# Optimization experiments

Measured on AMD Instinct MI355X. Metric: run time of the kernel, lower is better.

The kernel has to match this reference:

```python
import jax, jax.numpy as jnp
import numpy as np

B, D, H, W, C = 1, 6, 128, 128, 180
NH = 6
HD = C // NH
SCALE = HD ** -0.5
WS = (2, 8, 8)
SS = (1, 4, 4)
N = WS[0] * WS[1] * WS[2]  # 128 tokens per 3D window
HID = int(C * 2.0)  # GEGLU hidden = 360


def _rel_pos_index(ws):
    d, h, w = np.meshgrid(np.arange(ws[0]), np.arange(ws[1]), np.arange(ws[2]), indexing='ij')
    coords = np.stack([d, h, w]).reshape(3, -1)  # (3, N)
    rel = (coords[:, :, None] - coords[:, None, :]).transpose(1, 2, 0).astype(np.int64)
    rel[:, :, 0] += ws[0] - 1
    rel[:, :, 1] += ws[1] - 1
    rel[:, :, 2] += ws[2] - 1
    rel[:, :, 0] *= (2 * ws[1] - 1) * (2 * ws[2] - 1)
    rel[:, :, 1] *= (2 * ws[2] - 1)
    return rel.sum(-1).astype(np.int32)  # (N, N)


def _sine_pos(hw, nf, temperature=10000.0):
    scale = 2.0 * np.pi
    ones = np.ones((1, hw[0], hw[1]), np.float64)
    y = np.cumsum(ones, 1)
    x = np.cumsum(ones, 2)
    eps = 1e-6
    y = y / (y[:, -1:, :] + eps) * scale
    x = x / (x[:, :, -1:] + eps) * scale
    dim_t = temperature ** (2 * (np.arange(nf) // 2) / nf)
    px = x[..., None] / dim_t
    py = y[..., None] / dim_t
    px = np.stack([np.sin(px[..., 0::2]), np.cos(px[..., 1::2])], -1).reshape(1, hw[0], hw[1], -1)
    py = np.stack([np.sin(py[..., 0::2]), np.cos(py[..., 1::2])], -1).reshape(1, hw[0], hw[1], -1)
    pos = np.concatenate([py, px], -1)  # (1, H, W, 2*nf)
    return pos.reshape(1, hw[0] * hw[1], -1).astype(np.float32)


def _compute_mask():
    img = np.zeros((1, D, H, W, 1), np.float32)
    cnt = 0
    sl = lambda w, s: (slice(0, -w), slice(-w, -s), slice(-s, None))
    for ds in sl(WS[0], SS[0]):
        for hs in sl(WS[1], SS[1]):
            for ws_ in sl(WS[2], SS[2]):
                img[:, ds, hs, ws_, :] = cnt
                cnt += 1
    mw = img.reshape(1, D // WS[0], WS[0], H // WS[1], WS[1], W // WS[2], WS[2], 1)
    mw = mw.transpose(0, 1, 3, 5, 2, 4, 6, 7).reshape(-1, N)
    am = mw[:, None, :] - mw[:, :, None]
    return np.where(am != 0, -100.0, 0.0).astype(np.float32)  # (nW, N, N)


def win_part(x):
    b = x.shape[0]
    x = x.reshape(b, D // WS[0], WS[0], H // WS[1], WS[1], W // WS[2], WS[2], C)
    return x.transpose(0, 1, 3, 5, 2, 4, 6, 7).reshape(-1, N, C)


def win_rev(w, b):
    x = w.reshape(b, D // WS[0], H // WS[1], W // WS[2], WS[0], WS[1], WS[2], C)
    return x.transpose(0, 1, 4, 2, 5, 3, 6, 7).reshape(b, D, H, W, C)


def ln(x, g, b):
    m = x.mean(-1, keepdims=True)
    v = ((x - m) ** 2).mean(-1, keepdims=True)
    return (x - m) / jnp.sqrt(v + 1e-5) * g + b


def attn_fn(q, k, v, bias, mask):
    # q,k,v: (B_, NH, n, HD); bias: (NH, n, n) or None; mask: (nW, n, n) or None
    a = jnp.einsum('bhnd,bhmd->bhnm', q * SCALE, k)
    if bias is not None:
        a = a + bias[None]
    if mask is not None:
        nW = mask.shape[0]
        a = a.reshape(-1, nW, NH, a.shape[-2], a.shape[-1]) + mask[None, :, None]
        a = a.reshape(-1, NH, a.shape[-2], a.shape[-1])
    a = jax.nn.softmax(a, axis=-1)
    o = jnp.einsum('bhnm,bhmd->bhnd', a, v)
    return o.transpose(0, 2, 1, 3).reshape(o.shape[0], o.shape[2], -1)


def setup_inputs() -> dict:
    key = jax.random.key(0)
    ks = jax.random.split(key, 9)
    p = lambda k, shape: jax.random.normal(k, shape, jnp.float32) * 0.02
    return {
        'x': jax.random.normal(ks[0], (B, D, H, W, C), jnp.float32),
        'mask': jnp.asarray(_compute_mask()),
        'g1': jnp.ones((C,), jnp.float32), 'b1': jnp.zeros((C,), jnp.float32),
        'g2': jnp.ones((C,), jnp.float32), 'b2': jnp.zeros((C,), jnp.float32),
        'w_qkv_self': p(ks[1], (C, 3 * C)), 'b_qkv_self': jnp.zeros((3 * C,), jnp.float32),
        'w_qkv_mut': p(ks[2], (C, 3 * C)), 'b_qkv_mut': jnp.zeros((3 * C,), jnp.float32),
        'rpb_table': p(ks[3], ((2 * WS[0] - 1) * (2 * WS[1] - 1) * (2 * WS[2] - 1), NH)),
        'pos_bias': jnp.asarray(_sine_pos((WS[1], WS[2]), C // 2)),
        'w_proj': p(ks[4], (2 * C, C)), 'b_proj': jnp.zeros((C,), jnp.float32),
        'w_fc11': p(ks[5], (C, HID)), 'b_fc11': jnp.zeros((HID,), jnp.float32),
        'w_fc12': p(ks[6], (C, HID)), 'b_fc12': jnp.zeros((HID,), jnp.float32),
        'w_fc2': p(ks[7], (HID, C)), 'b_fc2': jnp.zeros((C,), jnp.float32),
        'rpi': jnp.asarray(_rel_pos_index(WS)),
    }


def reference(x, mask, g1, b1, g2, b2, w_qkv_self, b_qkv_self, w_qkv_mut, b_qkv_mut,
              rpb_table, pos_bias, w_proj, b_proj, w_fc11, b_fc11, w_fc12, b_fc12,
              w_fc2, b_fc2, rpi):
    # --- attention branch ---
    h = ln(x, g1, b1)
    h = jnp.roll(h, (-SS[0], -SS[1], -SS[2]), axis=(1, 2, 3))  # cyclic shift
    xw = win_part(h)  # (B*nW, N, C)
    B_ = xw.shape[0]

    def qkv(xin, wq, bq):
        t = (xin @ wq + bq).reshape(B_, -1, 3, NH, HD).transpose(2, 0, 3, 1, 4)
        return t[0], t[1], t[2]

    q, k, v = qkv(xw, w_qkv_self, b_qkv_self)
    bias = rpb_table[rpi.reshape(-1)].reshape(N, N, NH).transpose(2, 0, 1)
    x_self = attn_fn(q, k, v, bias, mask)

    # mutual attention between the two frames of each window
    pb = jnp.concatenate([pos_bias, pos_bias], axis=1)  # (1, N, C)
    qm, km, vm = qkv(xw + pb, w_qkv_mut, b_qkv_mut)
    half = N // 2
    q1, q2 = qm[:, :, :half], qm[:, :, half:]
    k1, k2 = km[:, :, :half], km[:, :, half:]
    v1, v2 = vm[:, :, :half], vm[:, :, half:]
    m2 = mask[:, :half, :half]
    x1 = attn_fn(q2, k1, v1, None, m2)
    x2 = attn_fn(q1, k2, v2, None, m2)
    xo = jnp.concatenate([jnp.concatenate([x1, x2], axis=1), x_self], axis=2)  # (B_, N, 2C)
    xo = xo @ w_proj + b_proj
    out = win_rev(xo, x.shape[0])
    out = jnp.roll(out, (SS[0], SS[1], SS[2]), axis=(1, 2, 3))
    x = x + out

    # --- GEGLU MLP branch ---
    h = ln(x, g2, b2)
    h = jax.nn.gelu(h @ w_fc11 + b_fc11, approximate=False) * (h @ w_fc12 + b_fc12)
    x = x + (h @ w_fc2 + b_fc2)
    return x
```

## Files before the change

### kernel.cpp

```cpp
#include <hip/hip_runtime.h>
#include <hip/hip_bf16.h>
#include <math.h>
#include <cstdio>


typedef __hip_bfloat16 bf16;
typedef __attribute__((ext_vector_type(8))) short short8;
typedef __attribute__((ext_vector_type(4))) unsigned short us4;
typedef __attribute__((ext_vector_type(4))) float f32x4;

#define SCALE_F 0.18257418583505536f
#define SZPE 18874368u

__device__ __forceinline__ bf16  f2b(float v){ return __float2bfloat16(v); }
__device__ __forceinline__ float bu2f(unsigned short u){
    union { unsigned int i; float f; } x; x.i = ((unsigned int)u) << 16; return x.f;
}
__device__ __forceinline__ f32x4 mfma16(short8 a, short8 b, f32x4 c){
    return __builtin_amdgcn_mfma_f32_16x16x32_bf16(a, b, c, 0, 0, 0);
}

__device__ __forceinline__ void gld16(const bf16* g, bf16* s){
    __builtin_amdgcn_global_load_lds(
        (const __attribute__((address_space(1))) unsigned int*)g,
        (__attribute__((address_space(3))) unsigned int*)s, 16, 0, 0);
}

__device__ __forceinline__ float gelu_erf(float x){
    float z  = fabsf(x) * 0.70710678118654752f;
    float t  = __builtin_amdgcn_rcpf(fmaf(0.3275911f, z, 1.f));
    float p  = fmaf(fmaf(fmaf(fmaf(1.061405429f, t, -1.453152027f),
                              t, 1.421413741f), t, -0.284496736f), t, 0.254829592f) * t;
    float e  = __expf(-z * z);
    float er = fmaf(-p, e, 1.f);
    er = (x >= 0.f) ? er : -er;
    return 0.5f * x * (1.f + er);
}

__device__ __forceinline__ int xswz(){
    return (blockIdx.x & 7) * ((int)gridDim.x >> 3) + ((int)blockIdx.x >> 3);
}

__device__ __forceinline__ int wincnt(int win, int tok){
    int d = (win >> 8) * 2 + (tok >> 6);
    int h = ((win >> 4) & 15) * 8 + ((tok >> 3) & 7);
    int w = (win & 15) * 8 + (tok & 7);
    int rd = (d >= 4) + (d >= 5);
    int rh = (h >= 120) + (h >= 124);
    int rw = (w >= 120) + (w >= 124);
    return (rd * 3 + rh) * 3 + rw;
}

__device__ __forceinline__ size_t wrev_base(int row){
    int win = row >> 7, tok = row & 127;
    int wd = win >> 8, wh = (win >> 4) & 15, ww = win & 15;
    int td = tok >> 6, th = (tok >> 3) & 7, tw = tok & 7;
    int d = wd * 2 + td + 1; if (d >= 6) d -= 6;
    int h = (wh * 8 + th + 4) & 127;
    int wcol = (ww * 8 + tw + 4) & 127;
    return ((size_t)((d * 128 + h) * 128 + wcol)) * 180;
}

__global__ __launch_bounds__(256) void k_pack_qkv(const float* __restrict__ w,
                                                  const float* __restrict__ bias,
                                                  bf16* __restrict__ Bt,
                                                  float* __restrict__ bb)
{
    int idx = blockIdx.x * 256 + threadIdx.x;
    int n = idx / 192, k = idx - n * 192;
    int three = n / 192;
    int rem = n - three * 192, nh = rem >> 5, hdp = rem & 31;
    int srcc = three * 180 + nh * 30 + hdp;
    float v = 0.f;
    if (hdp < 30 && k < 180) v = w[(size_t)k * 540 + srcc];
    if (three == 0) v *= SCALE_F;
    Bt[(size_t)n * 192 + k] = f2b(v);
    if (k == 0) bb[n] = (hdp < 30) ? ((three == 0 ? SCALE_F : 1.f) * bias[srcc]) : 0.f;
}

__global__ __launch_bounds__(256) void k_pack(const float* __restrict__ w,
                                              int NW, int K, int KP,
                                              bf16* __restrict__ Bt)
{
    int idx = blockIdx.x * 256 + threadIdx.x;
    int n = idx / KP, k = idx - n * KP;
    float v = (n < NW && k < K) ? w[(size_t)k * NW + n] : 0.f;
    Bt[idx] = f2b(v);
}

__global__ __launch_bounds__(256) void k_rpbg(const float* __restrict__ rpb,
                                              const int* __restrict__ rpi,
                                              bf16* __restrict__ biasrT)
{
    int n = blockIdx.x * 256 + threadIdx.x;
    int nh = n >> 14, rc = n & 16383;
    int row = rc >> 7, col = rc & 127;
    biasrT[((size_t)nh * 128 + col) * 128 + row] = f2b(rpb[rpi[rc] * 6 + nh]);
}

__global__ __launch_bounds__(256) void k_zpad(bf16* __restrict__ attn)
{
    int gi = blockIdx.x * 256 + threadIdx.x;
    int row = gi / 3, part = gi - row * 3;
    *(uint4*)&attn[(size_t)row * 384 + 360 + part * 8] = make_uint4(0u,0u,0u,0u);
}

template<bool ROLL_PB>
__global__ __launch_bounds__(256) void k_ln(const float* __restrict__ x,
                                            const float* __restrict__ g,
                                            const float* __restrict__ b,
                                            const float* __restrict__ pb,
                                            bf16* __restrict__ xw,
                                            bf16* __restrict__ xwm)
{
    int row  = blockIdx.x * 4 + (threadIdx.x >> 6);
    int lane = threadIdx.x & 63;
    const float* src;
    if (ROLL_PB) {
        src = x + wrev_base(row) - 0;
    } else {
        src = x + (size_t)row * 180;
    }
    float v0 = src[lane];
    float v1 = src[lane + 64];
    float v2 = (lane < 52) ? src[lane + 128] : 0.f;
    float s  = v0 + v1 + v2;
    float ss = v0*v0 + v1*v1 + v2*v2;
    #pragma unroll
    for (int o = 32; o > 0; o >>= 1) { s += __shfl_xor(s, o, 64); ss += __shfl_xor(ss, o, 64); }
    float mean = s * (1.f/180.f);
    float var  = ss * (1.f/180.f) - mean*mean;
    float rstd = rsqrtf(var + 1e-5f);

    bf16* dst = xw + (size_t)row * 192;
    float y0 = (v0-mean)*rstd*g[lane]     + b[lane];
    float y1 = (v1-mean)*rstd*g[lane+64]  + b[lane+64];
    float y2 = (lane < 52) ? ((v2-mean)*rstd*g[lane+128] + b[lane+128]) : 0.f;
    dst[lane]      = f2b(y0);
    dst[lane+64]   = f2b(y1);
    if (lane < 52) dst[lane+128] = f2b(y2);
    if (lane < 12) dst[180+lane] = f2b(0.f);
    if (ROLL_PB) {
        const float* pbr = pb + (size_t)(row & 63) * 180;
        bf16* dm = xwm + (size_t)row * 192;
        dm[lane]      = f2b(y0 + pbr[lane]);
        dm[lane+64]   = f2b(y1 + pbr[lane+64]);
        if (lane < 52) dm[lane+128] = f2b(y2 + pbr[lane+128]);
        if (lane < 12) dm[180+lane] = f2b(0.f);
    }
}

template<int KP, bool DUAL>
__device__ __forceinline__ void mm2(const bf16* __restrict__ A,
                                    const bf16* __restrict__ Bt1,
                                    const bf16* __restrict__ Bt2,
                                    bf16* As, bf16* Bs1, bf16* Bs2,
                                    int m0, int n0,
                                    f32x4 (&acc1)[2][4], f32x4 (&acc2)[2][4])
{
    const int tid = threadIdx.x;
    const int w = tid >> 6, l = tid & 63, q = l >> 4, c = l & 15;
    const int lr = l >> 3, lj = l & 7;
    const int swz = ((lj ^ lr) << 3);
    #pragma unroll
    for (int ks = 0; ks < KP / 64; ks++) {
        #pragma unroll
        for (int e = 0; e < 4; e++) {
            int m = (e * 4 + w) * 8 + lr;
            gld16(&A[(size_t)(m0 + m) * KP + ks * 64 + swz], &As[((e * 4 + w) * 8) * 64]);
        }
        #pragma unroll
        for (int e = 0; e < 2; e++) {
            int n = (e * 4 + w) * 8 + lr;
            gld16(&Bt1[(size_t)(n0 + n) * KP + ks * 64 + swz], &Bs1[((e * 4 + w) * 8) * 64]);
            if (DUAL)
                gld16(&Bt2[(size_t)(n0 + n) * KP + ks * 64 + swz], &Bs2[((e * 4 + w) * 8) * 64]);
        }
        __syncthreads();
        #pragma unroll
        for (int k32 = 0; k32 < 2; k32++) {
            int koff = (((k32 * 4 + q) ^ (c & 7)) << 3);
            short8 a[2];
            #pragma unroll
            for (int mt = 0; mt < 2; mt++)
                a[mt] = *(const short8*)&As[(w * 32 + mt * 16 + c) * 64 + koff];
            #pragma unroll
            for (int nt = 0; nt < 4; nt++) {
                short8 b1 = *(const short8*)&Bs1[(nt * 16 + c) * 64 + koff];
                #pragma unroll
                for (int mt = 0; mt < 2; mt++) acc1[mt][nt] = mfma16(a[mt], b1, acc1[mt][nt]);
                if (DUAL) {
                    short8 b2 = *(const short8*)&Bs2[(nt * 16 + c) * 64 + koff];
                    #pragma unroll
                    for (int mt = 0; mt < 2; mt++) acc2[mt][nt] = mfma16(a[mt], b2, acc2[mt][nt]);
                }
            }
        }
        __syncthreads();
    }
}

__device__ __forceinline__ int cs_idx(int row, int colt){
    return row * 64 + ((((colt >> 3) ^ ((row >> 2) & 7)) << 3) | (colt & 7));
}

__global__ __launch_bounds__(256) void k_qkv(const bf16* __restrict__ A,
                                             const bf16* __restrict__ Bt,
                                             const float* __restrict__ bb,
                                             bf16* __restrict__ outq)
{
    __shared__ __align__(16) bf16 As[128 * 64];
    __shared__ __align__(16) bf16 Bs[64 * 64];
    int bid = xswz();
    int n0 = (bid % 9) * 64, m0 = (bid / 9) * 128;
    f32x4 a1[2][4] = {}, a2[2][4];
    mm2<192, false>(A, Bt, nullptr, As, Bs, nullptr, m0, n0, a1, a2);

    int tid = threadIdx.x, w = tid >> 6, l = tid & 63, q = l >> 4, c = l & 15;
    bf16* Cs = As;
    #pragma unroll
    for (int mt = 0; mt < 2; mt++)
      #pragma unroll
      for (int nt = 0; nt < 4; nt++)
        #pragma unroll
        for (int r = 0; r < 4; r++) {
            int row = w * 32 + mt * 16 + q * 4 + r;
            int colt = nt * 16 + c;
            Cs[cs_idx(row, colt)] = f2b(a1[mt][nt][r] + bb[n0 + colt]);
        }
    __syncthreads();
    int win = m0 >> 7;
    #pragma unroll
    for (int e = 0; e < 4; e++) {
        int gi = e * 256 + tid;
        int row = gi >> 3, j = gi & 7, c8 = j * 8;
        int col = n0 + c8;
        int three = col / 192, rem = col - three * 192;
        int nh = rem >> 5, hdp = rem & 31;
        bf16* dst = outq + (size_t)three * SZPE + ((size_t)(win * 6 + nh) * 128 + row) * 32 + hdp;
        *(uint4*)dst = *(const uint4*)&Cs[row * 64 + ((j ^ ((row >> 2) & 7)) << 3)];
    }
}

__global__ __launch_bounds__(256) void k_proj(const bf16* __restrict__ A,
                                              const bf16* __restrict__ Bt,
                                              const float* __restrict__ bias,
                                              const float* __restrict__ xin,
                                              float* __restrict__ res)
{
    __shared__ __align__(16) char smem[24576];
    bf16*  As = (bf16*)smem;
    bf16*  Bs = (bf16*)(smem + 16384);
    float* Cs = (float*)smem;
    int bid = xswz();
    int n0 = (bid % 3) * 64, m0 = (bid / 3) * 128;
    f32x4 a1[2][4] = {}, a2[2][4];
    mm2<384, false>(A, Bt, nullptr, As, Bs, nullptr, m0, n0, a1, a2);

    int tid = threadIdx.x, w = tid >> 6, l = tid & 63, q = l >> 4, c = l & 15;
    #pragma unroll
    for (int h = 0; h < 2; h++) {
        __syncthreads();
        if ((w >> 1) == h) {
            #pragma unroll
            for (int mt = 0; mt < 2; mt++)
              #pragma unroll
              for (int nt = 0; nt < 4; nt++)
                #pragma unroll
                for (int r = 0; r < 4; r++) {
                    int rl = (w & 1) * 32 + mt * 16 + q * 4 + r;
                    Cs[rl * 76 + nt * 16 + c] = a1[mt][nt][r];
                }
        }
        __syncthreads();
        #pragma unroll
        for (int e = 0; e < 4; e++) {
            int slot = e * 256 + tid;
            int rl = slot >> 4, cq = slot & 15;
            int col = n0 + cq * 4;
            if (col < 180) {
                size_t base = wrev_base(m0 + h * 64 + rl) + col;
                float4 xi = *(const float4*)&xin[base];
                float4 bi = *(const float4*)&bias[col];
                const float* cp = &Cs[rl * 76 + cq * 4];
                float4 o;
                o.x = xi.x + cp[0] + bi.x;
                o.y = xi.y + cp[1] + bi.y;
                o.z = xi.z + cp[2] + bi.z;
                o.w = xi.w + cp[3] + bi.w;
                *(float4*)&res[base] = o;
            }
        }
    }
}

__global__ __launch_bounds__(256) void k_fc1(const bf16* __restrict__ A,
                                             const bf16* __restrict__ Bt1,
                                             const float* __restrict__ bb1,
                                             const bf16* __restrict__ Bt2,
                                             const float* __restrict__ bb2,
                                             bf16* __restrict__ hid)
{
    __shared__ __align__(16) bf16 As[128 * 64];
    __shared__ __align__(16) bf16 Bs1[64 * 64];
    __shared__ __align__(16) bf16 Bs2[64 * 64];
    int bid = xswz();
    int n0 = (bid % 6) * 64, m0 = (bid / 6) * 128;
    f32x4 a1[2][4] = {}, a2[2][4] = {};
    mm2<192, true>(A, Bt1, Bt2, As, Bs1, Bs2, m0, n0, a1, a2);

    int tid = threadIdx.x, w = tid >> 6, l = tid & 63, q = l >> 4, c = l & 15;
    bf16* Cs = As;
    #pragma unroll
    for (int mt = 0; mt < 2; mt++)
      #pragma unroll
      for (int nt = 0; nt < 4; nt++)
        #pragma unroll
        for (int r = 0; r < 4; r++) {
            int row = w * 32 + mt * 16 + q * 4 + r;
            int colt = nt * 16 + c;
            int col = n0 + colt;
            float hv = 0.f;
            if (col < 360)
                hv = gelu_erf(a1[mt][nt][r] + bb1[col]) * (a2[mt][nt][r] + bb2[col]);
            Cs[cs_idx(row, colt)] = f2b(hv);
        }
    __syncthreads();
    #pragma unroll
    for (int e = 0; e < 4; e++) {
        int gi = e * 256 + tid;
        int row = gi >> 3, j = gi & 7, c8 = j * 8;
        *(uint4*)&hid[(size_t)(m0 + row) * 384 + n0 + c8] =
            *(const uint4*)&Cs[row * 64 + ((j ^ ((row >> 2) & 7)) << 3)];
    }
}

__global__ __launch_bounds__(256) void k_fc2(const bf16* __restrict__ A,
                                             const bf16* __restrict__ Bt,
                                             const float* __restrict__ bias,
                                             float* __restrict__ out)
{
    __shared__ __align__(16) char smem[24576];
    bf16*  As = (bf16*)smem;
    bf16*  Bs = (bf16*)(smem + 16384);
    float* Cs = (float*)smem;
    int bid = xswz();
    int n0 = (bid % 3) * 64, m0 = (bid / 3) * 128;
    f32x4 a1[2][4] = {}, a2[2][4];
    mm2<384, false>(A, Bt, nullptr, As, Bs, nullptr, m0, n0, a1, a2);

    int tid = threadIdx.x, w = tid >> 6, l = tid & 63, q = l >> 4, c = l & 15;
    #pragma unroll
    for (int h = 0; h < 2; h++) {
        __syncthreads();
        if ((w >> 1) == h) {
            #pragma unroll
            for (int mt = 0; mt < 2; mt++)
              #pragma unroll
              for (int nt = 0; nt < 4; nt++)
                #pragma unroll
                for (int r = 0; r < 4; r++) {
                    int rl = (w & 1) * 32 + mt * 16 + q * 4 + r;
                    Cs[rl * 76 + nt * 16 + c] = a1[mt][nt][r];
                }
        }
        __syncthreads();
        #pragma unroll
        for (int e = 0; e < 4; e++) {
            int slot = e * 256 + tid;
            int rl = slot >> 4, cq = slot & 15;
            int col = n0 + cq * 4;
            if (col < 180) {
                size_t idx = (size_t)(m0 + h * 64 + rl) * 180 + col;
                float4 ov = *(const float4*)&out[idx];
                float4 bi = *(const float4*)&bias[col];
                const float* cp = &Cs[rl * 76 + cq * 4];
                ov.x += cp[0] + bi.x;
                ov.y += cp[1] + bi.y;
                ov.z += cp[2] + bi.z;
                ov.w += cp[3] + bi.w;
                *(float4*)&out[idx] = ov;
            }
        }
    }
}

template<bool MUT>
__global__ __launch_bounds__(256) void k_attn(const bf16* __restrict__ qkv,
                                              const bf16* __restrict__ biasrT,
                                              bf16* __restrict__ aout)
{
    __shared__ __align__(16) bf16 Vts[32 * 136];
    __shared__ __align__(16) bf16 Ps[128 * 136];

    int wh = blockIdx.x, win = wh / 6, nh = wh - win * 6;
    const bf16* qg = qkv + (size_t)wh * 4096;
    const bf16* kg = qg + (size_t)SZPE;
    const bf16* vg = qg + 2 * (size_t)SZPE;
    int tid = threadIdx.x, w = tid >> 6, l = tid & 63, q = l >> 4, c = l & 15;

    #pragma unroll
    for (int e = 0; e < 2; e++) {
        int base = (e * 256 + tid) * 8;
        int tok = base >> 5, hd0 = base & 31;
        uint4 vv = *(const uint4*)&vg[base];
        const bf16* pv = (const bf16*)&vv;
        #pragma unroll
        for (int i = 0; i < 8; i++) {
            int hd = hd0 + i;
            Vts[hd * 136 + (tok ^ (((hd >> 3) & 3) << 3))] = pv[i];
        }
    }

    f32x4 S[2][8];
    #pragma unroll
    for (int mt = 0; mt < 2; mt++)
        #pragma unroll
        for (int nt = 0; nt < 8; nt++) S[mt][nt] = (f32x4){0.f, 0.f, 0.f, 0.f};
    {
        short8 a[2];
        #pragma unroll
        for (int mt = 0; mt < 2; mt++) {
            int rq = w * 32 + mt * 16 + c;
            if (MUT) rq ^= 64;
            a[mt] = *(const short8*)&qg[rq * 32 + q * 8];
        }
        #pragma unroll
        for (int nt = 0; nt < 8; nt++) {
            short8 b = *(const short8*)&kg[(nt * 16 + c) * 32 + q * 8];
            #pragma unroll
            for (int mt = 0; mt < 2; mt++) S[mt][nt] = mfma16(a[mt], b, S[mt][nt]);
        }
    }

    int rcnt[2][4], ccnt[8];
    #pragma unroll
    for (int mt = 0; mt < 2; mt++)
        #pragma unroll
        for (int r = 0; r < 4; r++) {
            int row = w * 32 + mt * 16 + q * 4 + r;
            rcnt[mt][r] = wincnt(win, MUT ? (row & 63) : row);
        }
    #pragma unroll
    for (int nt = 0; nt < 8; nt++) {
        int col = nt * 16 + c;
        ccnt[nt] = wincnt(win, MUT ? (col & 63) : col);
    }

    float mx[2][4];
    #pragma unroll
    for (int mt = 0; mt < 2; mt++)
      #pragma unroll
      for (int r = 0; r < 4; r++) mx[mt][r] = -3.0e38f;

    #pragma unroll
    for (int mt = 0; mt < 2; mt++)
      #pragma unroll
      for (int nt = 0; nt < 8; nt++) {
        float bv[4];
        if (!MUT) {
            int col = nt * 16 + c;
            us4 bb = *(const us4*)&biasrT[((size_t)(nh * 128 + col)) * 128
                                          + w * 32 + mt * 16 + q * 4];
            #pragma unroll
            for (int r = 0; r < 4; r++) bv[r] = bu2f(bb[r]);
        }
        bool valid = (w < 2) == (nt < 4);
        #pragma unroll
        for (int r = 0; r < 4; r++) {
            float s = S[mt][nt][r];
            if (MUT) {
                s = (rcnt[mt][r] == ccnt[nt]) ? s : s - 100.f;
                s = valid ? s : -30000.f;
            } else {
                s += bv[r];
                if (rcnt[mt][r] != ccnt[nt]) s -= 100.f;
            }
            S[mt][nt][r] = s;
            mx[mt][r] = fmaxf(mx[mt][r], s);
        }
      }
    #pragma unroll
    for (int mt = 0; mt < 2; mt++)
      #pragma unroll
      for (int r = 0; r < 4; r++) {
          float m = mx[mt][r];
          #pragma unroll
          for (int o = 1; o < 16; o <<= 1) m = fmaxf(m, __shfl_xor(m, o, 64));
          mx[mt][r] = m;
      }

    float sm[2][4] = {};
    #pragma unroll
    for (int mt = 0; mt < 2; mt++)
      #pragma unroll
      for (int nt = 0; nt < 8; nt++)
        #pragma unroll
        for (int r = 0; r < 4; r++) {
            float p = __expf(S[mt][nt][r] - mx[mt][r]);
            sm[mt][r] += p;
            Ps[(w * 32 + mt * 16 + q * 4 + r) * 136 + ((nt * 16 + c) ^ (q << 3))] = f2b(p);
        }
    #pragma unroll
    for (int mt = 0; mt < 2; mt++)
      #pragma unroll
      for (int r = 0; r < 4; r++) {
          float s = sm[mt][r];
          #pragma unroll
          for (int o = 1; o < 16; o <<= 1) s += __shfl_xor(s, o, 64);
          sm[mt][r] = s;
      }
    __syncthreads();

    f32x4 O[2][2];
    #pragma unroll
    for (int mt = 0; mt < 2; mt++)
        #pragma unroll
        for (int nt = 0; nt < 2; nt++) O[mt][nt] = (f32x4){0.f, 0.f, 0.f, 0.f};
    #pragma unroll
    for (int ks = 0; ks < 4; ks++) {
        short8 a[2];
        #pragma unroll
        for (int mt = 0; mt < 2; mt++) {
            int row = w * 32 + mt * 16 + c;
            int xr = ((c >> 2) & 3) << 3;
            a[mt] = *(const short8*)&Ps[row * 136 + (ks * 32 + ((q << 3) ^ xr))];
        }
        #pragma unroll
        for (int nt = 0; nt < 2; nt++) {
            int hd = nt * 16 + c;
            int xv = ((hd >> 3) & 3) << 3;
            short8 b = *(const short8*)&Vts[hd * 136 + (ks * 32 + ((q << 3) ^ xv))];
            #pragma unroll
            for (int mt = 0; mt < 2; mt++) O[mt][nt] = mfma16(a[mt], b, O[mt][nt]);
        }
    }

    #pragma unroll
    for (int mt = 0; mt < 2; mt++)
      #pragma unroll
      for (int r = 0; r < 4; r++) {
          int row = w * 32 + mt * 16 + q * 4 + r;
          float inv = 1.f / sm[mt][r];
          #pragma unroll
          for (int nt = 0; nt < 2; nt++) {
              int col = nt * 16 + c;
              if (col < 30)
                  aout[((size_t)win * 128 + row) * 384 + (MUT ? 0 : 180) + nh * 30 + col] =
                      f2b(O[mt][nt][r] * inv);
          }
      }
}

extern "C" void kernel_launch(void* const* d_in, const int* in_sizes, int n_in,
                              void* d_out, int out_size, void* d_ws, size_t ws_size,
                              hipStream_t stream)
{
    const float* x     = (const float*)d_in[0];
    const float* mask  = (const float*)d_in[1];
    const float* g1    = (const float*)d_in[2];
    const float* b1    = (const float*)d_in[3];
    const float* g2    = (const float*)d_in[4];
    const float* b2    = (const float*)d_in[5];
    const float* wqs   = (const float*)d_in[6];
    const float* bqs   = (const float*)d_in[7];
    const float* wqm   = (const float*)d_in[8];
    const float* bqm   = (const float*)d_in[9];
    const float* rpb   = (const float*)d_in[10];
    const float* posb  = (const float*)d_in[11];
    const float* wproj = (const float*)d_in[12];
    const float* bproj = (const float*)d_in[13];
    const float* w11   = (const float*)d_in[14];
    const float* bf11  = (const float*)d_in[15];
    const float* w12   = (const float*)d_in[16];
    const float* bf12  = (const float*)d_in[17];
    const float* w2    = (const float*)d_in[18];
    const float* bf2   = (const float*)d_in[19];
    const int*   rpi   = (const int*)d_in[20];
    float* out = (float*)d_out;
    (void)mask;

    const size_t need = 265671168;
    if (ws_size < need) { fprintf(stderr, "[tmsa] ws too small: %zu < %zu\n", ws_size, need); return; }

    char* W = (char*)d_ws;
    bf16*  xw     = (bf16*)W;
    bf16*  xwm    = (bf16*)(W + 37748736);
    bf16*  attn   = (bf16*)(W + 75497472);
    bf16*  qkv    = (bf16*)(W + 150994944);
    bf16*  biasrT = (bf16*)(W + 264241152);
    bf16*  Btqs   = (bf16*)(W + 264634368);
    bf16*  Btqm   = (bf16*)(W + 264855552);
    float* bbqs   = (float*)(W + 265076736);
    float* bbqm   = (float*)(W + 265079040);
    bf16*  Btproj = (bf16*)(W + 265081344);
    bf16*  Btf11  = (bf16*)(W + 265228800);
    bf16*  Btf12  = (bf16*)(W + 265376256);
    bf16*  Btf2   = (bf16*)(W + 265523712);

    k_rpbg<<<dim3(384), 256, 0, stream>>>(rpb, rpi, biasrT);
    k_pack_qkv<<<dim3(432), 256, 0, stream>>>(wqs, bqs, Btqs, bbqs);
    k_pack_qkv<<<dim3(432), 256, 0, stream>>>(wqm, bqm, Btqm, bbqm);
    k_pack<<<dim3(288), 256, 0, stream>>>(wproj, 180, 360, 384, Btproj);
    k_pack<<<dim3(288), 256, 0, stream>>>(w11,   360, 180, 192, Btf11);
    k_pack<<<dim3(288), 256, 0, stream>>>(w12,   360, 180, 192, Btf12);
    k_pack<<<dim3(288), 256, 0, stream>>>(w2,    180, 360, 384, Btf2);

    k_ln<true><<<dim3(24576), 256, 0, stream>>>(x, g1, b1, posb, xw, xwm);
    k_zpad<<<dim3(1152), 256, 0, stream>>>(attn);
    k_qkv<<<dim3(6912), 256, 0, stream>>>(xw, Btqs, bbqs, qkv);
    k_attn<false><<<dim3(4608), 256, 0, stream>>>(qkv, biasrT, attn);
    k_qkv<<<dim3(6912), 256, 0, stream>>>(xwm, Btqm, bbqm, qkv);
    k_attn<true><<<dim3(4608), 256, 0, stream>>>(qkv, biasrT, attn);
    k_proj<<<dim3(2304), 256, 0, stream>>>(attn, Btproj, bproj, x, out);
    k_ln<false><<<dim3(24576), 256, 0, stream>>>(out, g2, b2, nullptr, xw, nullptr);
    k_fc1<<<dim3(4608), 256, 0, stream>>>(xw, Btf11, bf11, Btf12, bf12, attn);
    k_fc2<<<dim3(2304), 256, 0, stream>>>(attn, Btf2, bf2, out);
}
```

Baseline: 590.9 us.

## Load GEMM operands directly from global memory into MFMA registers, dropping LDS staging

The shared GEMM helper used by the qkv, proj, fc1 and fc2 kernels no longer stages A and B tiles through LDS with async global-to-LDS loads and barriers. Each lane now reads its MFMA fragments straight from global memory. This removes the block-wide barriers and frees LDS, which may allow more blocks per CU. In exchange, B tiles are re-read by all four waves and each read is a strided 16-byte access, so the kernels lean on L1/L2 hit rates instead of explicit data reuse.

```diff
diff --git a/kernel.cpp b/kernel.cpp
--- a/kernel.cpp
+++ b/kernel.cpp
@@ -18,12 +18,6 @@
 }
 __device__ __forceinline__ f32x4 mfma16(short8 a, short8 b, f32x4 c){
     return __builtin_amdgcn_mfma_f32_16x16x32_bf16(a, b, c, 0, 0, 0);
-}
-
-__device__ __forceinline__ void gld16(const bf16* g, bf16* s){
-    __builtin_amdgcn_global_load_lds(
-        (const __attribute__((address_space(1))) unsigned int*)g,
-        (__attribute__((address_space(3))) unsigned int*)s, 16, 0, 0);
 }
 
 __device__ __forceinline__ float gelu_erf(float x){
@@ -117,7 +111,7 @@
     int lane = threadIdx.x & 63;
     const float* src;
     if (ROLL_PB) {
-        src = x + wrev_base(row) - 0;
+        src = x + wrev_base(row);
     } else {
         src = x + (size_t)row * 180;
     }
@@ -151,52 +145,33 @@
 }
 
 template<int KP, bool DUAL>
-__device__ __forceinline__ void mm2(const bf16* __restrict__ A,
+__device__ __forceinline__ void mm3(const bf16* __restrict__ A,
                                     const bf16* __restrict__ Bt1,
                                     const bf16* __restrict__ Bt2,
-                                    bf16* As, bf16* Bs1, bf16* Bs2,
                                     int m0, int n0,
                                     f32x4 (&acc1)[2][4], f32x4 (&acc2)[2][4])
 {
     const int tid = threadIdx.x;
     const int w = tid >> 6, l = tid & 63, q = l >> 4, c = l & 15;
-    const int lr = l >> 3, lj = l & 7;
-    const int swz = ((lj ^ lr) << 3);
-    #pragma unroll
-    for (int ks = 0; ks < KP / 64; ks++) {
-        #pragma unroll
-        for (int e = 0; e < 4; e++) {
-            int m = (e * 4 + w) * 8 + lr;
-            gld16(&A[(size_t)(m0 + m) * KP + ks * 64 + swz], &As[((e * 4 + w) * 8) * 64]);
-        }
-        #pragma unroll
-        for (int e = 0; e < 2; e++) {
-            int n = (e * 4 + w) * 8 + lr;
-            gld16(&Bt1[(size_t)(n0 + n) * KP + ks * 64 + swz], &Bs1[((e * 4 + w) * 8) * 64]);
-            if (DUAL)
-                gld16(&Bt2[(size_t)(n0 + n) * KP + ks * 64 + swz], &Bs2[((e * 4 + w) * 8) * 64]);
-        }
-        __syncthreads();
-        #pragma unroll
-        for (int k32 = 0; k32 < 2; k32++) {
-            int koff = (((k32 * 4 + q) ^ (c & 7)) << 3);
-            short8 a[2];
-            #pragma unroll
-            for (int mt = 0; mt < 2; mt++)
-                a[mt] = *(const short8*)&As[(w * 32 + mt * 16 + c) * 64 + koff];
-            #pragma unroll
-            for (int nt = 0; nt < 4; nt++) {
-                short8 b1 = *(const short8*)&Bs1[(nt * 16 + c) * 64 + koff];
-                #pragma unroll
-                for (int mt = 0; mt < 2; mt++) acc1[mt][nt] = mfma16(a[mt], b1, acc1[mt][nt]);
-                if (DUAL) {
-                    short8 b2 = *(const short8*)&Bs2[(nt * 16 + c) * 64 + koff];
-                    #pragma unroll
-                    for (int mt = 0; mt < 2; mt++) acc2[mt][nt] = mfma16(a[mt], b2, acc2[mt][nt]);
-                }
+    const bf16* a0p = A + (size_t)(m0 + w * 32 + c) * KP + q * 8;
+    const bf16* a1p = a0p + (size_t)16 * KP;
+    const bf16* bp  = Bt1 + (size_t)(n0 + c) * KP + q * 8;
+    const bf16* b2p = DUAL ? (Bt2 + (size_t)(n0 + c) * KP + q * 8) : nullptr;
+    #pragma unroll
+    for (int ks = 0; ks < KP / 32; ks++) {
+        short8 a0 = *(const short8*)(a0p + ks * 32);
+        short8 a1 = *(const short8*)(a1p + ks * 32);
+        #pragma unroll
+        for (int nt = 0; nt < 4; nt++) {
+            short8 b1 = *(const short8*)(bp + (size_t)(nt * 16) * KP + ks * 32);
+            acc1[0][nt] = mfma16(a0, b1, acc1[0][nt]);
+            acc1[1][nt] = mfma16(a1, b1, acc1[1][nt]);
+            if (DUAL) {
+                short8 b2 = *(const short8*)(b2p + (size_t)(nt * 16) * KP + ks * 32);
+                acc2[0][nt] = mfma16(a0, b2, acc2[0][nt]);
+                acc2[1][nt] = mfma16(a1, b2, acc2[1][nt]);
             }
         }
-        __syncthreads();
     }
 }
 
@@ -209,15 +184,13 @@
                                              const float* __restrict__ bb,
                                              bf16* __restrict__ outq)
 {
-    __shared__ __align__(16) bf16 As[128 * 64];
-    __shared__ __align__(16) bf16 Bs[64 * 64];
+    __shared__ __align__(16) bf16 Cs[128 * 64];
     int bid = xswz();
     int n0 = (bid % 9) * 64, m0 = (bid / 9) * 128;
     f32x4 a1[2][4] = {}, a2[2][4];
-    mm2<192, false>(A, Bt, nullptr, As, Bs, nullptr, m0, n0, a1, a2);
+    mm3<192, false>(A, Bt, nullptr, m0, n0, a1, a2);
 
     int tid = threadIdx.x, w = tid >> 6, l = tid & 63, q = l >> 4, c = l & 15;
-    bf16* Cs = As;
     #pragma unroll
     for (int mt = 0; mt < 2; mt++)
       #pragma unroll
@@ -248,14 +221,11 @@
                                               const float* __restrict__ xin,
                                               float* __restrict__ res)
 {
-    __shared__ __align__(16) char smem[24576];
-    bf16*  As = (bf16*)smem;
-    bf16*  Bs = (bf16*)(smem + 16384);
-    float* Cs = (float*)smem;
+    __shared__ __align__(16) float Cs[64 * 76];
     int bid = xswz();
     int n0 = (bid % 3) * 64, m0 = (bid / 3) * 128;
     f32x4 a1[2][4] = {}, a2[2][4];
-    mm2<384, false>(A, Bt, nullptr, As, Bs, nullptr, m0, n0, a1, a2);
+    mm3<384, false>(A, Bt, nullptr, m0, n0, a1, a2);
 
     int tid = threadIdx.x, w = tid >> 6, l = tid & 63, q = l >> 4, c = l & 15;
     #pragma unroll
@@ -301,16 +271,13 @@
                                              const float* __restrict__ bb2,
                                              bf16* __restrict__ hid)
 {
-    __shared__ __align__(16) bf16 As[128 * 64];
-    __shared__ __align__(16) bf16 Bs1[64 * 64];
-    __shared__ __align__(16) bf16 Bs2[64 * 64];
+    __shared__ __align__(16) bf16 Cs[128 * 64];
     int bid = xswz();
     int n0 = (bid % 6) * 64, m0 = (bid / 6) * 128;
     f32x4 a1[2][4] = {}, a2[2][4] = {};
-    mm2<192, true>(A, Bt1, Bt2, As, Bs1, Bs2, m0, n0, a1, a2);
+    mm3<192, true>(A, Bt1, Bt2, m0, n0, a1, a2);
 
     int tid = threadIdx.x, w = tid >> 6, l = tid & 63, q = l >> 4, c = l & 15;
-    bf16* Cs = As;
     #pragma unroll
     for (int mt = 0; mt < 2; mt++)
       #pragma unroll
@@ -340,14 +307,11 @@
                                              const float* __restrict__ bias,
                                              float* __restrict__ out)
 {
-    __shared__ __align__(16) char smem[24576];
-    bf16*  As = (bf16*)smem;
-    bf16*  Bs = (bf16*)(smem + 16384);
-    float* Cs = (float*)smem;
+    __shared__ __align__(16) float Cs[64 * 76];
     int bid = xswz();
     int n0 = (bid % 3) * 64, m0 = (bid / 3) * 128;
     f32x4 a1[2][4] = {}, a2[2][4];
-    mm2<384, false>(A, Bt, nullptr, As, Bs, nullptr, m0, n0, a1, a2);
+    mm3<384, false>(A, Bt, nullptr, m0, n0, a1, a2);
 
     int tid = threadIdx.x, w = tid >> 6, l = tid & 63, q = l >> 4, c = l & 15;
     #pragma unroll
```

After: 901.3 us. 1.53x slower.

## Double GEMM M-tile to 256 rows and vectorize layernorm loads/stores

Applied to the files above, without the earlier changes.

All four GEMM kernels (qkv, proj, fc1, fc2) now use 256-row tiles. Each wave computes 64 rows with a 4x4 MFMA accumulator grid, so each B tile loaded into LDS is reused across twice as many rows and the grid size is halved. The layernorm kernel switches to float4 loads and packed 4-wide bf16 stores instead of scalar per-lane accesses. The larger tiles raise register and LDS use (fc1 has dual 4x4 accumulators), which may reduce occupancy and latency hiding.

```diff
diff --git a/kernel.cpp b/kernel.cpp
--- a/kernel.cpp
+++ b/kernel.cpp
@@ -15,6 +15,13 @@
 __device__ __forceinline__ bf16  f2b(float v){ return __float2bfloat16(v); }
 __device__ __forceinline__ float bu2f(unsigned short u){
     union { unsigned int i; float f; } x; x.i = ((unsigned int)u) << 16; return x.f;
+}
+__device__ __forceinline__ us4 pack4(float a, float b, float c, float d){
+    us4 r;
+    bf16 t0 = f2b(a), t1 = f2b(b), t2 = f2b(c), t3 = f2b(d);
+    r[0] = *(unsigned short*)&t0; r[1] = *(unsigned short*)&t1;
+    r[2] = *(unsigned short*)&t2; r[3] = *(unsigned short*)&t3;
+    return r;
 }
 __device__ __forceinline__ f32x4 mfma16(short8 a, short8 b, f32x4 c){
     return __builtin_amdgcn_mfma_f32_16x16x32_bf16(a, b, c, 0, 0, 0);
@@ -115,17 +122,11 @@
 {
     int row  = blockIdx.x * 4 + (threadIdx.x >> 6);
     int lane = threadIdx.x & 63;
-    const float* src;
-    if (ROLL_PB) {
-        src = x + wrev_base(row) - 0;
-    } else {
-        src = x + (size_t)row * 180;
-    }
-    float v0 = src[lane];
-    float v1 = src[lane + 64];
-    float v2 = (lane < 52) ? src[lane + 128] : 0.f;
-    float s  = v0 + v1 + v2;
-    float ss = v0*v0 + v1*v1 + v2*v2;
+    const float* src = ROLL_PB ? (x + wrev_base(row)) : (x + (size_t)row * 180);
+    float4 v = make_float4(0.f, 0.f, 0.f, 0.f);
+    if (lane < 45) v = *(const float4*)&src[lane * 4];
+    float s  = v.x + v.y + v.z + v.w;
+    float ss = v.x*v.x + v.y*v.y + v.z*v.z + v.w*v.w;
     #pragma unroll
     for (int o = 32; o > 0; o >>= 1) { s += __shfl_xor(s, o, 64); ss += __shfl_xor(ss, o, 64); }
     float mean = s * (1.f/180.f);
@@ -133,30 +134,37 @@
     float rstd = rsqrtf(var + 1e-5f);
 
     bf16* dst = xw + (size_t)row * 192;
-    float y0 = (v0-mean)*rstd*g[lane]     + b[lane];
-    float y1 = (v1-mean)*rstd*g[lane+64]  + b[lane+64];
-    float y2 = (lane < 52) ? ((v2-mean)*rstd*g[lane+128] + b[lane+128]) : 0.f;
-    dst[lane]      = f2b(y0);
-    dst[lane+64]   = f2b(y1);
-    if (lane < 52) dst[lane+128] = f2b(y2);
-    if (lane < 12) dst[180+lane] = f2b(0.f);
+    float4 y = make_float4(0.f, 0.f, 0.f, 0.f);
+    if (lane < 45) {
+        float4 gv = *(const float4*)&g[lane * 4];
+        float4 bv = *(const float4*)&b[lane * 4];
+        y.x = (v.x - mean) * rstd * gv.x + bv.x;
+        y.y = (v.y - mean) * rstd * gv.y + bv.y;
+        y.z = (v.z - mean) * rstd * gv.z + bv.z;
+        y.w = (v.w - mean) * rstd * gv.w + bv.w;
+        *(us4*)&dst[lane * 4] = pack4(y.x, y.y, y.z, y.w);
+    } else if (lane < 48) {
+        *(us4*)&dst[lane * 4] = (us4){0, 0, 0, 0};
+    }
     if (ROLL_PB) {
-        const float* pbr = pb + (size_t)(row & 63) * 180;
         bf16* dm = xwm + (size_t)row * 192;
-        dm[lane]      = f2b(y0 + pbr[lane]);
-        dm[lane+64]   = f2b(y1 + pbr[lane+64]);
-        if (lane < 52) dm[lane+128] = f2b(y2 + pbr[lane+128]);
-        if (lane < 12) dm[180+lane] = f2b(0.f);
+        if (lane < 45) {
+            const float* pbr = pb + (size_t)(row & 63) * 180;
+            float4 pv = *(const float4*)&pbr[lane * 4];
+            *(us4*)&dm[lane * 4] = pack4(y.x + pv.x, y.y + pv.y, y.z + pv.z, y.w + pv.w);
+        } else if (lane < 48) {
+            *(us4*)&dm[lane * 4] = (us4){0, 0, 0, 0};
+        }
     }
 }
 
 template<int KP, bool DUAL>
-__device__ __forceinline__ void mm2(const bf16* __restrict__ A,
+__device__ __forceinline__ void mm4(const bf16* __restrict__ A,
                                     const bf16* __restrict__ Bt1,
                                     const bf16* __restrict__ Bt2,
                                     bf16* As, bf16* Bs1, bf16* Bs2,
                                     int m0, int n0,
-                                    f32x4 (&acc1)[2][4], f32x4 (&acc2)[2][4])
+                                    f32x4 (&acc1)[4][4], f32x4 (&acc2)[4][4])
 {
     const int tid = threadIdx.x;
     const int w = tid >> 6, l = tid & 63, q = l >> 4, c = l & 15;
@@ -165,7 +173,7 @@
     #pragma unroll
     for (int ks = 0; ks < KP / 64; ks++) {
         #pragma unroll
-        for (int e = 0; e < 4; e++) {
+        for (int e = 0; e < 8; e++) {
             int m = (e * 4 + w) * 8 + lr;
             gld16(&A[(size_t)(m0 + m) * KP + ks * 64 + swz], &As[((e * 4 + w) * 8) * 64]);
         }
@@ -180,19 +188,19 @@
         #pragma unroll
         for (int k32 = 0; k32 < 2; k32++) {
             int koff = (((k32 * 4 + q) ^ (c & 7)) << 3);
-            short8 a[2];
+            short8 a[4];
             #pragma unroll
-            for (int mt = 0; mt < 2; mt++)
-                a[mt] = *(const short8*)&As[(w * 32 + mt * 16 + c) * 64 + koff];
+            for (int mt = 0; mt < 4; mt++)
+                a[mt] = *(const short8*)&As[(w * 64 + mt * 16 + c) * 64 + koff];
             #pragma unroll
             for (int nt = 0; nt < 4; nt++) {
                 short8 b1 = *(const short8*)&Bs1[(nt * 16 + c) * 64 + koff];
                 #pragma unroll
-                for (int mt = 0; mt < 2; mt++) acc1[mt][nt] = mfma16(a[mt], b1, acc1[mt][nt]);
+                for (int mt = 0; mt < 4; mt++) acc1[mt][nt] = mfma16(a[mt], b1, acc1[mt][nt]);
                 if (DUAL) {
                     short8 b2 = *(const short8*)&Bs2[(nt * 16 + c) * 64 + koff];
                     #pragma unroll
-                    for (int mt = 0; mt < 2; mt++) acc2[mt][nt] = mfma16(a[mt], b2, acc2[mt][nt]);
+                    for (int mt = 0; mt < 4; mt++) acc2[mt][nt] = mfma16(a[mt], b2, acc2[mt][nt]);
                 }
             }
         }
@@ -209,35 +217,35 @@
                                              const float* __restrict__ bb,
                                              bf16* __restrict__ outq)
 {
-    __shared__ __align__(16) bf16 As[128 * 64];
+    __shared__ __align__(16) bf16 As[256 * 64];
     __shared__ __align__(16) bf16 Bs[64 * 64];
     int bid = xswz();
-    int n0 = (bid % 9) * 64, m0 = (bid / 9) * 128;
-    f32x4 a1[2][4] = {}, a2[2][4];
-    mm2<192, false>(A, Bt, nullptr, As, Bs, nullptr, m0, n0, a1, a2);
+    int n0 = (bid % 9) * 64, m0 = (bid / 9) * 256;
+    f32x4 a1[4][4] = {}, a2[4][4];
+    mm4<192, false>(A, Bt, nullptr, As, Bs, nullptr, m0, n0, a1, a2);
 
     int tid = threadIdx.x, w = tid >> 6, l = tid & 63, q = l >> 4, c = l & 15;
     bf16* Cs = As;
     #pragma unroll
-    for (int mt = 0; mt < 2; mt++)
+    for (int mt = 0; mt < 4; mt++)
       #pragma unroll
       for (int nt = 0; nt < 4; nt++)
         #pragma unroll
         for (int r = 0; r < 4; r++) {
-            int row = w * 32 + mt * 16 + q * 4 + r;
+            int row = w * 64 + mt * 16 + q * 4 + r;
             int colt = nt * 16 + c;
             Cs[cs_idx(row, colt)] = f2b(a1[mt][nt][r] + bb[n0 + colt]);
         }
     __syncthreads();
-    int win = m0 >> 7;
-    #pragma unroll
-    for (int e = 0; e < 4; e++) {
+    #pragma unroll
+    for (int e = 0; e < 8; e++) {
         int gi = e * 256 + tid;
         int row = gi >> 3, j = gi & 7, c8 = j * 8;
         int col = n0 + c8;
         int three = col / 192, rem = col - three * 192;
         int nh = rem >> 5, hdp = rem & 31;
-        bf16* dst = outq + (size_t)three * SZPE + ((size_t)(win * 6 + nh) * 128 + row) * 32 + hdp;
+        int gr = m0 + row, win = gr >> 7, rw = gr & 127;
+        bf16* dst = outq + (size_t)three * SZPE + ((size_t)(win * 6 + nh) * 128 + rw) * 32 + hdp;
         *(uint4*)dst = *(const uint4*)&Cs[row * 64 + ((j ^ ((row >> 2) & 7)) << 3)];
     }
 }
@@ -248,27 +256,27 @@
                                               const float* __restrict__ xin,
                                               float* __restrict__ res)
 {
-    __shared__ __align__(16) char smem[24576];
+    __shared__ __align__(16) char smem[40960];
     bf16*  As = (bf16*)smem;
-    bf16*  Bs = (bf16*)(smem + 16384);
+    bf16*  Bs = (bf16*)(smem + 32768);
     float* Cs = (float*)smem;
     int bid = xswz();
-    int n0 = (bid % 3) * 64, m0 = (bid / 3) * 128;
-    f32x4 a1[2][4] = {}, a2[2][4];
-    mm2<384, false>(A, Bt, nullptr, As, Bs, nullptr, m0, n0, a1, a2);
+    int n0 = (bid % 3) * 64, m0 = (bid / 3) * 256;
+    f32x4 a1[4][4] = {}, a2[4][4];
+    mm4<384, false>(A, Bt, nullptr, As, Bs, nullptr, m0, n0, a1, a2);
 
     int tid = threadIdx.x, w = tid >> 6, l = tid & 63, q = l >> 4, c = l & 15;
     #pragma unroll
-    for (int h = 0; h < 2; h++) {
+    for (int h = 0; h < 4; h++) {
         __syncthreads();
-        if ((w >> 1) == h) {
+        if (w == h) {
             #pragma unroll
-            for (int mt = 0; mt < 2; mt++)
+            for (int mt = 0; mt < 4; mt++)
               #pragma unroll
               for (int nt = 0; nt < 4; nt++)
                 #pragma unroll
                 for (int r = 0; r < 4; r++) {
-                    int rl = (w & 1) * 32 + mt * 16 + q * 4 + r;
+                    int rl = mt * 16 + q * 4 + r;
                     Cs[rl * 76 + nt * 16 + c] = a1[mt][nt][r];
                 }
         }
@@ -301,23 +309,23 @@
                                              const float* __restrict__ bb2,
                                              bf16* __restrict__ hid)
 {
-    __shared__ __align__(16) bf16 As[128 * 64];
+    __shared__ __align__(16) bf16 As[256 * 64];
     __shared__ __align__(16) bf16 Bs1[64 * 64];
     __shared__ __align__(16) bf16 Bs2[64 * 64];
     int bid = xswz();
-    int n0 = (bid % 6) * 64, m0 = (bid / 6) * 128;
-    f32x4 a1[2][4] = {}, a2[2][4] = {};
-    mm2<192, true>(A, Bt1, Bt2, As, Bs1, Bs2, m0, n0, a1, a2);
+    int n0 = (bid % 6) * 64, m0 = (bid / 6) * 256;
+    f32x4 a1[4][4] = {}, a2[4][4] = {};
+    mm4<192, true>(A, Bt1, Bt2, As, Bs1, Bs2, m0, n0, a1, a2);
 
     int tid = threadIdx.x, w = tid >> 6, l = tid & 63, q = l >> 4, c = l & 15;
     bf16* Cs = As;
     #pragma unroll
-    for (int mt = 0; mt < 2; mt++)
+    for (int mt = 0; mt < 4; mt++)
       #pragma unroll
       for (int nt = 0; nt < 4; nt++)
         #pragma unroll
         for (int r = 0; r < 4; r++) {
-            int row = w * 32 + mt * 16 + q * 4 + r;
+            int row = w * 64 + mt * 16 + q * 4 + r;
             int colt = nt * 16 + c;
             int col = n0 + colt;
             float hv = 0.f;
@@ -327,7 +335,7 @@
         }
     __syncthreads();
     #pragma unroll
-    for (int e = 0; e < 4; e++) {
+    for (int e = 0; e < 8; e++) {
         int gi = e * 256 + tid;
         int row = gi >> 3, j = gi & 7, c8 = j * 8;
         *(uint4*)&hid[(size_t)(m0 + row) * 384 + n0 + c8] =
@@ -340,27 +348,27 @@
                                              const float* __restrict__ bias,
                                              float* __restrict__ out)
 {
-    __shared__ __align__(16) char smem[24576];
+    __shared__ __align__(16) char smem[40960];
     bf16*  As = (bf16*)smem;
-    bf16*  Bs = (bf16*)(smem + 16384);
+    bf16*  Bs = (bf16*)(smem + 32768);
     float* Cs = (float*)smem;
     int bid = xswz();
-    int n0 = (bid % 3) * 64, m0 = (bid / 3) * 128;
-    f32x4 a1[2][4] = {}, a2[2][4];
-    mm2<384, false>(A, Bt, nullptr, As, Bs, nullptr, m0, n0, a1, a2);
+    int n0 = (bid % 3) * 64, m0 = (bid / 3) * 256;
+    f32x4 a1[4][4] = {}, a2[4][4];
+    mm4<384, false>(A, Bt, nullptr, As, Bs, nullptr, m0, n0, a1, a2);
 
     int tid = threadIdx.x, w = tid >> 6, l = tid & 63, q = l >> 4, c = l & 15;
     #pragma unroll
-    for (int h = 0; h < 2; h++) {
+    for (int h = 0; h < 4; h++) {
         __syncthreads();
-        if ((w >> 1) == h) {
+        if (w == h) {
             #pragma unroll
-            for (int mt = 0; mt < 2; mt++)
+            for (int mt = 0; mt < 4; mt++)
               #pragma unroll
               for (int nt = 0; nt < 4; nt++)
                 #pragma unroll
                 for (int r = 0; r < 4; r++) {
-                    int rl = (w & 1) * 32 + mt * 16 + q * 4 + r;
+                    int rl = mt * 16 + q * 4 + r;
                     Cs[rl * 76 + nt * 16 + c] = a1[mt][nt][r];
                 }
         }
@@ -608,12 +616,12 @@
 
     k_ln<true><<<dim3(24576), 256, 0, stream>>>(x, g1, b1, posb, xw, xwm);
     k_zpad<<<dim3(1152), 256, 0, stream>>>(attn);
-    k_qkv<<<dim3(6912), 256, 0, stream>>>(xw, Btqs, bbqs, qkv);
+    k_qkv<<<dim3(3456), 256, 0, stream>>>(xw, Btqs, bbqs, qkv);
     k_attn<false><<<dim3(4608), 256, 0, stream>>>(qkv, biasrT, attn);
-    k_qkv<<<dim3(6912), 256, 0, stream>>>(xwm, Btqm, bbqm, qkv);
+    k_qkv<<<dim3(3456), 256, 0, stream>>>(xwm, Btqm, bbqm, qkv);
     k_attn<true><<<dim3(4608), 256, 0, stream>>>(qkv, biasrT, attn);
-    k_proj<<<dim3(2304), 256, 0, stream>>>(attn, Btproj, bproj, x, out);
+    k_proj<<<dim3(1152), 256, 0, stream>>>(attn, Btproj, bproj, x, out);
     k_ln<false><<<dim3(24576), 256, 0, stream>>>(out, g2, b2, nullptr, xw, nullptr);
-    k_fc1<<<dim3(4608), 256, 0, stream>>>(xw, Btf11, bf11, Btf12, bf12, attn);
-    k_fc2<<<dim3(2304), 256, 0, stream>>>(attn, Btf2, bf2, out);
-}
+    k_fc1<<<dim3(2304), 256, 0, stream>>>(xw, Btf11, bf11, Btf12, bf12, attn);
+    k_fc2<<<dim3(1152), 256, 0, stream>>>(attn, Btf2, bf2, out);
+}
```

Result: slower. 610.0 us (+3.2%).
